# Optimization experiments

Measured on AMD Instinct MI355X. Metric: run time of the kernel, lower is better.

## Reference

```python
import jax, jax.numpy as jnp
import numpy as np

N_NODES = 50000
N_EDGES = 800000
IN_FEATS = 128
HIDDEN = 128
OUT_FEATS = 2
NUM_GRAPHS = 100


def xavier(key, shape):
    fan_in, fan_out = shape[1], shape[0]
    a = jnp.sqrt(6.0 / (fan_in + fan_out))
    return jax.random.uniform(key, shape, jnp.float32, -a, a)


def setup_inputs() -> dict:
    key = jax.random.key(0)
    ks = jax.random.split(key, 10)
    x = jax.random.normal(ks[0], (N_NODES, IN_FEATS), jnp.float32)
    edge_index = jax.random.randint(ks[1], (2, N_EDGES), 0, N_NODES, jnp.int64)
    edge_weight = jax.random.uniform(ks[2], (N_EDGES,), jnp.float32)
    batch = jnp.sort(jax.random.randint(ks[3], (N_NODES,), 0, NUM_GRAPHS, jnp.int64))
    return {
        "x": x,
        "edge_index": edge_index,
        "edge_weight": edge_weight,
        "batch": batch,
        "W1": xavier(ks[4], (HIDDEN, IN_FEATS)),
        "b1": jnp.zeros((HIDDEN,), jnp.float32),
        "W2": xavier(ks[5], (HIDDEN, HIDDEN)),
        "b2": jnp.zeros((HIDDEN,), jnp.float32),
        "lin1_w": xavier(ks[6], (IN_FEATS, HIDDEN)),
        "lin1_b": jnp.zeros((IN_FEATS,), jnp.float32),
        "lin2_w": xavier(ks[7], (OUT_FEATS, IN_FEATS)),
        "lin2_b": jnp.zeros((OUT_FEATS,), jnp.float32),
    }


def gcn_conv(x, row, col, ew, W, b, n_nodes):
    # PyG GCNConv: symmetric normalization with self-loops already included
    # deg[i] = sum of edge weights into node i
    deg = jax.ops.segment_sum(ew, col, num_segments=n_nodes)
    dinv = jnp.where(deg > 0, jax.lax.rsqrt(deg), 0.0)
    norm = dinv[row] * ew * dinv[col]                      # [E]
    h = x @ W.T                                            # [N, out]
    msg = norm[:, None] * h[row]                           # [E, out]
    out = jax.ops.segment_sum(msg, col, num_segments=n_nodes)
    return out + b


def reference(x, edge_index, edge_weight, batch, W1, b1, W2, b2,
              lin1_w, lin1_b, lin2_w, lin2_b):
    n = x.shape[0]
    # add self-loops with weight 1 (PyG default fill_value=1.0)
    loops = jnp.arange(n, dtype=edge_index.dtype)
    row = jnp.concatenate([edge_index[0], loops])
    col = jnp.concatenate([edge_index[1], loops])
    ew = jnp.concatenate([edge_weight, jnp.ones((n,), edge_weight.dtype)])

    h = jax.nn.relu(gcn_conv(x, row, col, ew, W1, b1, n))
    h = jax.nn.relu(gcn_conv(h, row, col, ew, W2, b2, n))

    # global_mean_pool over graph ids
    sums = jax.ops.segment_sum(h, batch, num_segments=NUM_GRAPHS)
    cnt = jax.ops.segment_sum(jnp.ones((n,), h.dtype), batch, num_segments=NUM_GRAPHS)
    g = sums / jnp.maximum(cnt, 1.0)[:, None]              # [G, hidden]

    # dropout is identity in eval mode
    g = jax.nn.relu(g @ lin1_w.T + lin1_b)
    return g @ lin2_w.T + lin2_b
```

## Files before the change

### kernel.cpp

```cpp
#include <hip/hip_runtime.h>


typedef unsigned long long ull;
typedef short bf16x8 __attribute__((ext_vector_type(8)));
typedef float f32x4 __attribute__((ext_vector_type(4)));

#define BCAP 2560
#define TILE_E 2048
#define NBINS 512

__device__ inline ushort f2bf(float f) {
    unsigned u = __float_as_uint(f);
    unsigned r = (u + 0x7FFF + ((u >> 16) & 1)) >> 16;
    return (ushort)r;
}
__device__ inline void bsplit(float f, ushort& h, ushort& l) {
    h = f2bf(f);
    float hf = __uint_as_float(((unsigned)h) << 16);
    l = f2bf(f - hf);
}
__device__ inline float bflo(unsigned g) { return __uint_as_float(g << 16); }
__device__ inline float bfhi(unsigned g) { return __uint_as_float(g & 0xffff0000u); }

__global__ void k_wsplit(const float* __restrict__ W1, const float* __restrict__ W2,
                         ushort* __restrict__ w1hi, ushort* __restrict__ w1lo,
                         ushort* __restrict__ w2hi, ushort* __restrict__ w2lo,
                         unsigned* __restrict__ cursor) {
    int i = blockIdx.x * blockDim.x + threadIdx.x;
    if (i < NBINS) cursor[i] = 0;
    if (i < 4096) {
        float4 v = ((const float4*)W1)[i];
        ushort4 h, l;
        bsplit(v.x, h.x, l.x); bsplit(v.y, h.y, l.y);
        bsplit(v.z, h.z, l.z); bsplit(v.w, h.w, l.w);
        ((ushort4*)w1hi)[i] = h; ((ushort4*)w1lo)[i] = l;
    } else if (i < 8192) {
        int j = i - 4096;
        float4 v = ((const float4*)W2)[j];
        ushort4 h, l;
        bsplit(v.x, h.x, l.x); bsplit(v.y, h.y, l.y);
        bsplit(v.z, h.z, l.z); bsplit(v.w, h.w, l.w);
        ((ushort4*)w2hi)[j] = h; ((ushort4*)w2lo)[j] = l;
    }
}

template <int AFP32, int POOL>
__device__ __forceinline__ void gemm_body(int blk, int t,
                                          const void* __restrict__ Xsrc,
                                          const ushort* __restrict__ whi,
                                          const ushort* __restrict__ wlo,
                                          ushort* __restrict__ Y, int N,
                                          const int* __restrict__ batch,
                                          const float* __restrict__ bias,
                                          float* __restrict__ pooled) {
    int lane = t & 63;
    int wave = t >> 6;
    int quad = lane >> 4;
    int l16  = lane & 15;
    int rowbase = blk * 128 + wave * 32;

    const f32x4 zero = {0.f, 0.f, 0.f, 0.f};
    f32x4 acc[2][8];
#pragma unroll
    for (int i = 0; i < 2; ++i)
#pragma unroll
        for (int j = 0; j < 8; ++j) acc[i][j] = zero;

#pragma unroll
    for (int kc = 0; kc < 128; kc += 32) {
        bf16x8 ah[2];
#pragma unroll
        for (int rt = 0; rt < 2; ++rt) {
            int r0 = rowbase + rt * 16 + l16;
            r0 = r0 < N ? r0 : N - 1;
            if (AFP32) {
                const float* ap = (const float*)Xsrc + (size_t)r0 * 128 + kc + quad * 8;
                float4 a0 = *(const float4*)ap;
                float4 a1 = *(const float4*)(ap + 4);
                bf16x8 v;
                v[0] = (short)f2bf(a0.x); v[1] = (short)f2bf(a0.y);
                v[2] = (short)f2bf(a0.z); v[3] = (short)f2bf(a0.w);
                v[4] = (short)f2bf(a1.x); v[5] = (short)f2bf(a1.y);
                v[6] = (short)f2bf(a1.z); v[7] = (short)f2bf(a1.w);
                ah[rt] = v;
            } else {
                ah[rt] = *(const bf16x8*)((const ushort*)Xsrc + (size_t)r0 * 128 + kc + quad * 8);
            }
        }
#pragma unroll
        for (int ct = 0; ct < 8; ++ct) {
            int boff = (ct * 16 + l16) * 128 + kc + quad * 8;
            bf16x8 bh = *(const bf16x8*)(whi + boff);
            bf16x8 bl = *(const bf16x8*)(wlo + boff);
#pragma unroll
            for (int rt = 0; rt < 2; ++rt) {
                acc[rt][ct] = __builtin_amdgcn_mfma_f32_16x16x32_bf16(ah[rt], bh, acc[rt][ct], 0, 0, 0);
                acc[rt][ct] = __builtin_amdgcn_mfma_f32_16x16x32_bf16(ah[rt], bl, acc[rt][ct], 0, 0, 0);
            }
        }
    }
    if constexpr (!POOL) {
#pragma unroll
        for (int rt = 0; rt < 2; ++rt) {
#pragma unroll
            for (int r = 0; r < 4; ++r) {
                int rowi = rowbase + rt * 16 + quad * 4 + r;
                if (rowi < N) {
                    ushort* yp = Y + (size_t)rowi * 128 + l16;
#pragma unroll
                    for (int ct = 0; ct < 8; ++ct)
                        yp[ct * 16] = f2bf(acc[rt][ct][r]);
                }
            }
        }
    } else {
        __shared__ ushort hb[128][132];
        __shared__ int bs[128];
        int n0 = blk * 128;
        if (t < 128) bs[t] = (n0 + t < N) ? batch[n0 + t] : -1;
#pragma unroll
        for (int ct = 0; ct < 8; ++ct) {
            float bb = bias[ct * 16 + l16];
#pragma unroll
            for (int rt = 0; rt < 2; ++rt)
#pragma unroll
                for (int r = 0; r < 4; ++r) {
                    int rl = wave * 32 + rt * 16 + quad * 4 + r;
                    hb[rl][ct * 16 + l16] = f2bf(fmaxf(acc[rt][ct][r] + bb, 0.f));
                }
        }
        __syncthreads();
        int col = t & 127, half = t >> 7;
        float a = 0.f; int cur = -2;
        for (int r = 0; r < 64; ++r) {
            int row = half * 64 + r;
            int g = bs[row];
            if (g != cur) {
                if (cur >= 0) atomicAdd(&pooled[cur * 128 + col], a);
                a = 0.f; cur = g;
            }
            if (g >= 0) a += __uint_as_float(((unsigned)hb[row][col]) << 16);
        }
        if (cur >= 0) atomicAdd(&pooled[cur * 128 + col], a);
    }
}

__global__ __launch_bounds__(256, 4) void k_front(const float* __restrict__ x,
                                                  const ushort* __restrict__ w1hi,
                                                  const ushort* __restrict__ w1lo,
                                                  ushort* __restrict__ h1, int N, int gb,
                                                  const int* __restrict__ row,
                                                  const int* __restrict__ col,
                                                  const float* __restrict__ ew,
                                                  ull* __restrict__ edata,
                                                  unsigned* __restrict__ cursor, int E) {
    __shared__ unsigned hist[NBINS];
    __shared__ unsigned gbase[NBINS];
    int b = blockIdx.x;
    if (b < gb) {
        gemm_body<1, 0>(b, threadIdx.x, x, w1hi, w1lo, h1, N, nullptr, nullptr, nullptr);
        return;
    }
    int t = threadIdx.x;
    int e0 = (b - gb) * TILE_E;
    hist[t] = 0; hist[t + 256] = 0;
    __syncthreads();
    int cl[TILE_E / 256];
#pragma unroll
    for (int i = 0; i < TILE_E / 256; ++i) {
        int e = e0 + i * 256 + t;
        int c = e < E ? col[e] : -1;
        cl[i] = c;
        if (c >= 0) atomicAdd(&hist[c >> 7], 1u);
    }
    __syncthreads();
#pragma unroll
    for (int i = 0; i < 2; ++i) {
        int bin = t + i * 256;
        unsigned h = hist[bin];
        if (h) gbase[bin] = atomicAdd(&cursor[bin], h);
    }
    __syncthreads();
#pragma unroll
    for (int i = 0; i < TILE_E / 256; ++i) {
        int c = cl[i];
        if (c < 0) continue;
        int e = e0 + i * 256 + t;
        unsigned q = (unsigned)rintf(ew[e] * 32768.0f);
        if (q > 32767u) q = 32767u;
        unsigned val = (q << 17) | (unsigned)row[e];
        int bk = c >> 7;
        unsigned off = atomicSub(&hist[bk], 1u) - 1u;
        unsigned dst = gbase[bk] + off;
        if (dst < (unsigned)BCAP)
            edata[(size_t)bk * BCAP + dst] = ((ull)(unsigned)c << 32) | (ull)val;
    }
}

__global__ __launch_bounds__(256) void k_slots(const ull* __restrict__ edata,
                                               const unsigned* __restrict__ cursor,
                                               ull* __restrict__ packed,
                                               unsigned* __restrict__ slots, int N) {
    __shared__ unsigned cnt[128];
    __shared__ unsigned ews[128];
    int b = blockIdx.x, t = threadIdx.x;
    if (t < 128) { cnt[t] = 0; ews[t] = 0; }
    __syncthreads();
    unsigned m = cursor[b];
    if (m > (unsigned)BCAP) m = BCAP;
    const ull* ed = edata + (size_t)b * BCAP;
    for (unsigned k = t; k < m; k += 256) {
        ull pv = ed[k];
        unsigned c = (unsigned)(pv >> 32);
        unsigned val = (unsigned)pv;
        unsigned clc = c & 127u;
        unsigned pos = atomicAdd(&cnt[clc], 1u);
        if (pos < 64u) slots[((size_t)c << 6) + pos] = val;
        atomicAdd(&ews[clc], val >> 17);
    }
    __syncthreads();
    if (t < 128) {
        int node = b * 128 + t;
        if (node < N) packed[node] = ((ull)cnt[t] << 32) | (ull)ews[t];
    }
}

__global__ __launch_bounds__(256, 4) void k_gemm2pool(const ushort* __restrict__ X,
                                                      const ushort* __restrict__ whi,
                                                      const ushort* __restrict__ wlo,
                                                      const int* __restrict__ batch,
                                                      const float* __restrict__ bias,
                                                      float* __restrict__ pooled, int N) {
    gemm_body<0, 1>(blockIdx.x, threadIdx.x, X, whi, wlo, nullptr, N, batch, bias, pooled);
}

template <int RELU>
__global__ __launch_bounds__(256) void k_agg(const ushort* __restrict__ H,
                                             ushort* __restrict__ Ob,
                                             const ull* __restrict__ packed,
                                             const unsigned* __restrict__ slots,
                                             const float* __restrict__ bias, int N) {
    int wid = __builtin_amdgcn_readfirstlane((blockIdx.x * blockDim.x + threadIdx.x) >> 6);
    int lane = threadIdx.x & 63;
    if (wid >= N) return;
    const unsigned* HU = (const unsigned*)H;
    const unsigned* PU = (const unsigned*)packed;
    const float kq = 3.0517578125e-5f;
    ull pk = packed[wid];
    int cnt = (int)(pk >> 32); cnt = cnt < 64 ? cnt : 64;
    float dsum = (float)(unsigned)(pk & 0xffffffffull) * kq;
    float dc = rsqrtf(1.0f + dsum);
    float dcs = dc * kq;
    const unsigned* SL = slots + ((size_t)wid << 6);
    unsigned gss = HU[(size_t)wid * 64 + lane];
    float ax = dc * dc * bflo(gss), ay = dc * dc * bfhi(gss);
    int c1 = cnt - 1;
    for (int j = 0; j < cnt; j += 8) {
        int j1 = j+1 < c1 ? j+1 : c1, j2 = j+2 < c1 ? j+2 : c1, j3 = j+3 < c1 ? j+3 : c1;
        int j4 = j+4 < c1 ? j+4 : c1, j5 = j+5 < c1 ? j+5 : c1, j6 = j+6 < c1 ? j+6 : c1;
        int j7 = j+7 < c1 ? j+7 : c1;
        unsigned p0 = SL[j],  p1 = SL[j1], p2 = SL[j2], p3 = SL[j3];
        unsigned p4 = SL[j4], p5 = SL[j5], p6 = SL[j6], p7 = SL[j7];
        unsigned s0 = p0 & 0x1FFFFu, s1 = p1 & 0x1FFFFu, s2 = p2 & 0x1FFFFu, s3 = p3 & 0x1FFFFu;
        unsigned s4 = p4 & 0x1FFFFu, s5 = p5 & 0x1FFFFu, s6 = p6 & 0x1FFFFu, s7 = p7 & 0x1FFFFu;
        float q0 = (float)(p0 >> 17);
        float q1 = j+1 < cnt ? (float)(p1 >> 17) : 0.f;
        float q2 = j+2 < cnt ? (float)(p2 >> 17) : 0.f;
        float q3 = j+3 < cnt ? (float)(p3 >> 17) : 0.f;
        float q4 = j+4 < cnt ? (float)(p4 >> 17) : 0.f;
        float q5 = j+5 < cnt ? (float)(p5 >> 17) : 0.f;
        float q6 = j+6 < cnt ? (float)(p6 >> 17) : 0.f;
        float q7 = j+7 < cnt ? (float)(p7 >> 17) : 0.f;
        float d0 = rsqrtf(1.f + (float)PU[2*s0] * kq);
        float d1 = rsqrtf(1.f + (float)PU[2*s1] * kq);
        float d2 = rsqrtf(1.f + (float)PU[2*s2] * kq);
        float d3 = rsqrtf(1.f + (float)PU[2*s3] * kq);
        float d4 = rsqrtf(1.f + (float)PU[2*s4] * kq);
        float d5 = rsqrtf(1.f + (float)PU[2*s5] * kq);
        float d6 = rsqrtf(1.f + (float)PU[2*s6] * kq);
        float d7 = rsqrtf(1.f + (float)PU[2*s7] * kq);
        float w0 = d0 * q0 * dcs, w1 = d1 * q1 * dcs, w2 = d2 * q2 * dcs, w3 = d3 * q3 * dcs;
        float w4 = d4 * q4 * dcs, w5 = d5 * q5 * dcs, w6 = d6 * q6 * dcs, w7 = d7 * q7 * dcs;
        unsigned g0 = HU[(size_t)s0 * 64 + lane];
        unsigned g1 = HU[(size_t)s1 * 64 + lane];
        unsigned g2 = HU[(size_t)s2 * 64 + lane];
        unsigned g3 = HU[(size_t)s3 * 64 + lane];
        unsigned g4 = HU[(size_t)s4 * 64 + lane];
        unsigned g5 = HU[(size_t)s5 * 64 + lane];
        unsigned g6 = HU[(size_t)s6 * 64 + lane];
        unsigned g7 = HU[(size_t)s7 * 64 + lane];
        ax += w0 * bflo(g0); ay += w0 * bfhi(g0);
        ax += w1 * bflo(g1); ay += w1 * bfhi(g1);
        ax += w2 * bflo(g2); ay += w2 * bfhi(g2);
        ax += w3 * bflo(g3); ay += w3 * bfhi(g3);
        ax += w4 * bflo(g4); ay += w4 * bfhi(g4);
        ax += w5 * bflo(g5); ay += w5 * bfhi(g5);
        ax += w6 * bflo(g6); ay += w6 * bfhi(g6);
        ax += w7 * bflo(g7); ay += w7 * bfhi(g7);
    }
    if constexpr (RELU) {
        float2 bb = ((const float2*)bias)[lane];
        ax = fmaxf(ax + bb.x, 0.f);
        ay = fmaxf(ay + bb.y, 0.f);
    }
    unsigned pkout = (unsigned)f2bf(ax) | ((unsigned)f2bf(ay) << 16);
    ((unsigned*)Ob)[(size_t)wid * 64 + lane] = pkout;
}

__global__ __launch_bounds__(128) void k_mlp(const float* __restrict__ pooled,
                                             const int* __restrict__ batch,
                                             const float* __restrict__ w1,
                                             const float* __restrict__ b1,
                                             const float* __restrict__ w2,
                                             const float* __restrict__ b2,
                                             float* __restrict__ out, int N, int G) {
    __shared__ float pl[128];
    __shared__ float h1[128];
    int g = blockIdx.x, t = threadIdx.x;
    int lo = 0, hi = N;
    while (lo < hi) { int m = (lo + hi) >> 1; if (batch[m] < g) lo = m + 1; else hi = m; }
    int s = lo;
    lo = s; hi = N;
    while (lo < hi) { int m = (lo + hi) >> 1; if (batch[m] < g + 1) lo = m + 1; else hi = m; }
    float cnt = (float)(lo - s);
    pl[t] = pooled[g * 128 + t] / fmaxf(cnt, 1.0f);
    __syncthreads();
    float sum = b1[t];
#pragma unroll 4
    for (int k = 0; k < 128; ++k) sum += w1[t * 128 + k] * pl[k];
    h1[t] = fmaxf(sum, 0.f);
    __syncthreads();
    if (t < 2) {
        float s2 = b2[t];
        for (int k = 0; k < 128; ++k) s2 += w2[t * 128 + k] * h1[k];
        out[g * 2 + t] = s2;
    }
}

extern "C" void kernel_launch(void* const* d_in, const int* in_sizes, int n_in,
                              void* d_out, int out_size, void* d_ws, size_t ws_size,
                              hipStream_t stream) {
    const float* x   = (const float*)d_in[0];
    const int*   ei  = (const int*)d_in[1];
    const float* ew  = (const float*)d_in[2];
    const int* batch = (const int*)d_in[3];
    const float* W1  = (const float*)d_in[4];
    const float* b1  = (const float*)d_in[5];
    const float* W2  = (const float*)d_in[6];
    const float* b2  = (const float*)d_in[7];
    const float* l1w = (const float*)d_in[8];
    const float* l1b = (const float*)d_in[9];
    const float* l2w = (const float*)d_in[10];
    const float* l2b = (const float*)d_in[11];
    float* out = (float*)d_out;

    const int E = in_sizes[2];
    const int N = in_sizes[3];
    const int G = out_size / 2;
    const int Npad = (N + 127) & ~127;
    const int nbk = (N + 127) >> 7;
    const int* row = ei;
    const int* col = ei + E;

    char* p = (char*)d_ws;
    auto alloc = [&](size_t bytes) -> void* {
        void* r = (void*)p;
        p += (bytes + 511) & ~(size_t)511;
        return r;
    };
    ull*     packed = (ull*)alloc((size_t)N * 8);
    unsigned* slots = (unsigned*)alloc((size_t)N * 64 * 4);
    ushort* w1hi  = (ushort*)alloc(16384 * 2);
    ushort* w1lo  = (ushort*)alloc(16384 * 2);
    ushort* w2hi  = (ushort*)alloc(16384 * 2);
    ushort* w2lo  = (ushort*)alloc(16384 * 2);
    ushort* h1    = (ushort*)alloc((size_t)Npad * 128 * 2);
    ushort* hagg  = (ushort*)alloc((size_t)Npad * 128 * 2);
    float* pooled = (float*)alloc((size_t)G * 128 * 4);
    ull*   edata  = (ull*)alloc((size_t)nbk * BCAP * 8);
    unsigned* cursor = (unsigned*)alloc(NBINS * 4);

    hipMemsetAsync(pooled, 0, (size_t)G * 128 * 4, stream);

    int nbS = (E + TILE_E - 1) / TILE_E;
    int gb = Npad / 128;
    int ab = ((size_t)N * 64 + 255) / 256;
    k_wsplit<<<32, 256, 0, stream>>>(W1, W2, w1hi, w1lo, w2hi, w2lo, cursor);
    k_front<<<gb + nbS, 256, 0, stream>>>(x, w1hi, w1lo, h1, N, gb,
                                          row, col, ew, edata, cursor, E);
    k_slots<<<nbk, 256, 0, stream>>>(edata, cursor, packed, slots, N);
    k_agg<1><<<ab, 256, 0, stream>>>(h1, hagg, packed, slots, b1, N);
    k_agg<0><<<ab, 256, 0, stream>>>(hagg, h1, packed, slots, nullptr, N);
    k_gemm2pool<<<gb, 256, 0, stream>>>(h1, w2hi, w2lo, batch, b2, pooled, N);
    k_mlp<<<G, 128, 0, stream>>>(pooled, batch, l1w, l1b, l2w, l2b, out, N, G);
}
```

Measured before the change: 237.8 us.

## Fuse second aggregation with GEMM2 and pooling; split weights inline

Merges the second aggregation pass, the second GEMM, the bias/ReLU step and mean-pool accumulation into one kernel. Aggregated rows are staged in an LDS tile and fed straight to MFMA, so the intermediate h1 round trip through global memory goes away. The weight split kernel is removed and each GEMM now splits fp32 weights into bf16 hi/lo inline, and the cursor reset is folded into the pooled memset. This cuts two launches and one global write/read of N×128 activations, but adds redundant per-block weight conversion work and gives the aggregation phase less parallelism (one wave handles 16 nodes serially).

Result: slower. 261.1 us (+9.8%).

```diff
diff --git a/kernel.cpp b/kernel.cpp
--- a/kernel.cpp
+++ b/kernel.cpp
@@ -8,6 +8,7 @@
 #define BCAP 2560
 #define TILE_E 2048
 #define NBINS 512
+#define APAD 136
 
 __device__ inline ushort f2bf(float f) {
     unsigned u = __float_as_uint(f);
@@ -22,37 +23,24 @@
 __device__ inline float bflo(unsigned g) { return __uint_as_float(g << 16); }
 __device__ inline float bfhi(unsigned g) { return __uint_as_float(g & 0xffff0000u); }
 
-__global__ void k_wsplit(const float* __restrict__ W1, const float* __restrict__ W2,
-                         ushort* __restrict__ w1hi, ushort* __restrict__ w1lo,
-                         ushort* __restrict__ w2hi, ushort* __restrict__ w2lo,
-                         unsigned* __restrict__ cursor) {
-    int i = blockIdx.x * blockDim.x + threadIdx.x;
-    if (i < NBINS) cursor[i] = 0;
-    if (i < 4096) {
-        float4 v = ((const float4*)W1)[i];
-        ushort4 h, l;
-        bsplit(v.x, h.x, l.x); bsplit(v.y, h.y, l.y);
-        bsplit(v.z, h.z, l.z); bsplit(v.w, h.w, l.w);
-        ((ushort4*)w1hi)[i] = h; ((ushort4*)w1lo)[i] = l;
-    } else if (i < 8192) {
-        int j = i - 4096;
-        float4 v = ((const float4*)W2)[j];
-        ushort4 h, l;
-        bsplit(v.x, h.x, l.x); bsplit(v.y, h.y, l.y);
-        bsplit(v.z, h.z, l.z); bsplit(v.w, h.w, l.w);
-        ((ushort4*)w2hi)[j] = h; ((ushort4*)w2lo)[j] = l;
-    }
-}
-
-template <int AFP32, int POOL>
-__device__ __forceinline__ void gemm_body(int blk, int t,
-                                          const void* __restrict__ Xsrc,
-                                          const ushort* __restrict__ whi,
-                                          const ushort* __restrict__ wlo,
-                                          ushort* __restrict__ Y, int N,
-                                          const int* __restrict__ batch,
-                                          const float* __restrict__ bias,
-                                          float* __restrict__ pooled) {
+__device__ __forceinline__ void wfrag(const float* __restrict__ wp, bf16x8& bh, bf16x8& bl) {
+    float4 w0 = *(const float4*)wp;
+    float4 w1 = *(const float4*)(wp + 4);
+    ushort h, l;
+    bsplit(w0.x, h, l); bh[0] = (short)h; bl[0] = (short)l;
+    bsplit(w0.y, h, l); bh[1] = (short)h; bl[1] = (short)l;
+    bsplit(w0.z, h, l); bh[2] = (short)h; bl[2] = (short)l;
+    bsplit(w0.w, h, l); bh[3] = (short)h; bl[3] = (short)l;
+    bsplit(w1.x, h, l); bh[4] = (short)h; bl[4] = (short)l;
+    bsplit(w1.y, h, l); bh[5] = (short)h; bl[5] = (short)l;
+    bsplit(w1.z, h, l); bh[6] = (short)h; bl[6] = (short)l;
+    bsplit(w1.w, h, l); bh[7] = (short)h; bl[7] = (short)l;
+}
+
+__device__ __forceinline__ void gemm1_body(int blk, int t,
+                                           const float* __restrict__ X,
+                                           const float* __restrict__ W,
+                                           ushort* __restrict__ Y, int N) {
     int lane = t & 63;
     int wave = t >> 6;
     int quad = lane >> 4;
@@ -73,25 +61,20 @@
         for (int rt = 0; rt < 2; ++rt) {
             int r0 = rowbase + rt * 16 + l16;
             r0 = r0 < N ? r0 : N - 1;
-            if (AFP32) {
-                const float* ap = (const float*)Xsrc + (size_t)r0 * 128 + kc + quad * 8;
-                float4 a0 = *(const float4*)ap;
-                float4 a1 = *(const float4*)(ap + 4);
-                bf16x8 v;
-                v[0] = (short)f2bf(a0.x); v[1] = (short)f2bf(a0.y);
-                v[2] = (short)f2bf(a0.z); v[3] = (short)f2bf(a0.w);
-                v[4] = (short)f2bf(a1.x); v[5] = (short)f2bf(a1.y);
-                v[6] = (short)f2bf(a1.z); v[7] = (short)f2bf(a1.w);
-                ah[rt] = v;
-            } else {
-                ah[rt] = *(const bf16x8*)((const ushort*)Xsrc + (size_t)r0 * 128 + kc + quad * 8);
-            }
+            const float* ap = X + (size_t)r0 * 128 + kc + quad * 8;
+            float4 a0 = *(const float4*)ap;
+            float4 a1 = *(const float4*)(ap + 4);
+            bf16x8 v;
+            v[0] = (short)f2bf(a0.x); v[1] = (short)f2bf(a0.y);
+            v[2] = (short)f2bf(a0.z); v[3] = (short)f2bf(a0.w);
+            v[4] = (short)f2bf(a1.x); v[5] = (short)f2bf(a1.y);
+            v[6] = (short)f2bf(a1.z); v[7] = (short)f2bf(a1.w);
+            ah[rt] = v;
         }
 #pragma unroll
         for (int ct = 0; ct < 8; ++ct) {
-            int boff = (ct * 16 + l16) * 128 + kc + quad * 8;
-            bf16x8 bh = *(const bf16x8*)(whi + boff);
-            bf16x8 bl = *(const bf16x8*)(wlo + boff);
+            bf16x8 bh, bl;
+            wfrag(W + (size_t)(ct * 16 + l16) * 128 + kc + quad * 8, bh, bl);
 #pragma unroll
             for (int rt = 0; rt < 2; ++rt) {
                 acc[rt][ct] = __builtin_amdgcn_mfma_f32_16x16x32_bf16(ah[rt], bh, acc[rt][ct], 0, 0, 0);
@@ -99,55 +82,23 @@
             }
         }
     }
-    if constexpr (!POOL) {
-#pragma unroll
-        for (int rt = 0; rt < 2; ++rt) {
-#pragma unroll
-            for (int r = 0; r < 4; ++r) {
-                int rowi = rowbase + rt * 16 + quad * 4 + r;
-                if (rowi < N) {
-                    ushort* yp = Y + (size_t)rowi * 128 + l16;
-#pragma unroll
-                    for (int ct = 0; ct < 8; ++ct)
-                        yp[ct * 16] = f2bf(acc[rt][ct][r]);
-                }
+#pragma unroll
+    for (int rt = 0; rt < 2; ++rt) {
+#pragma unroll
+        for (int r = 0; r < 4; ++r) {
+            int rowi = rowbase + rt * 16 + quad * 4 + r;
+            if (rowi < N) {
+                ushort* yp = Y + (size_t)rowi * 128 + l16;
+#pragma unroll
+                for (int ct = 0; ct < 8; ++ct)
+                    yp[ct * 16] = f2bf(acc[rt][ct][r]);
             }
         }
-    } else {
-        __shared__ ushort hb[128][132];
-        __shared__ int bs[128];
-        int n0 = blk * 128;
-        if (t < 128) bs[t] = (n0 + t < N) ? batch[n0 + t] : -1;
-#pragma unroll
-        for (int ct = 0; ct < 8; ++ct) {
-            float bb = bias[ct * 16 + l16];
-#pragma unroll
-            for (int rt = 0; rt < 2; ++rt)
-#pragma unroll
-                for (int r = 0; r < 4; ++r) {
-                    int rl = wave * 32 + rt * 16 + quad * 4 + r;
-                    hb[rl][ct * 16 + l16] = f2bf(fmaxf(acc[rt][ct][r] + bb, 0.f));
-                }
-        }
-        __syncthreads();
-        int col = t & 127, half = t >> 7;
-        float a = 0.f; int cur = -2;
-        for (int r = 0; r < 64; ++r) {
-            int row = half * 64 + r;
-            int g = bs[row];
-            if (g != cur) {
-                if (cur >= 0) atomicAdd(&pooled[cur * 128 + col], a);
-                a = 0.f; cur = g;
-            }
-            if (g >= 0) a += __uint_as_float(((unsigned)hb[row][col]) << 16);
-        }
-        if (cur >= 0) atomicAdd(&pooled[cur * 128 + col], a);
     }
 }
 
 __global__ __launch_bounds__(256, 4) void k_front(const float* __restrict__ x,
-                                                  const ushort* __restrict__ w1hi,
-                                                  const ushort* __restrict__ w1lo,
+                                                  const float* __restrict__ W1,
                                                   ushort* __restrict__ h1, int N, int gb,
                                                   const int* __restrict__ row,
                                                   const int* __restrict__ col,
@@ -158,7 +109,7 @@
     __shared__ unsigned gbase[NBINS];
     int b = blockIdx.x;
     if (b < gb) {
-        gemm_body<1, 0>(b, threadIdx.x, x, w1hi, w1lo, h1, N, nullptr, nullptr, nullptr);
+        gemm1_body(b, threadIdx.x, x, W1, h1, N);
         return;
     }
     int t = threadIdx.x;
@@ -225,26 +176,12 @@
     }
 }
 
-__global__ __launch_bounds__(256, 4) void k_gemm2pool(const ushort* __restrict__ X,
-                                                      const ushort* __restrict__ whi,
-                                                      const ushort* __restrict__ wlo,
-                                                      const int* __restrict__ batch,
-                                                      const float* __restrict__ bias,
-                                                      float* __restrict__ pooled, int N) {
-    gemm_body<0, 1>(blockIdx.x, threadIdx.x, X, whi, wlo, nullptr, N, batch, bias, pooled);
-}
-
-template <int RELU>
-__global__ __launch_bounds__(256) void k_agg(const ushort* __restrict__ H,
-                                             ushort* __restrict__ Ob,
-                                             const ull* __restrict__ packed,
-                                             const unsigned* __restrict__ slots,
-                                             const float* __restrict__ bias, int N) {
-    int wid = __builtin_amdgcn_readfirstlane((blockIdx.x * blockDim.x + threadIdx.x) >> 6);
-    int lane = threadIdx.x & 63;
-    if (wid >= N) return;
-    const unsigned* HU = (const unsigned*)H;
-    const unsigned* PU = (const unsigned*)packed;
+__device__ __forceinline__ void agg_node(int wid, int lane,
+                                         const unsigned* __restrict__ HU,
+                                         const unsigned* __restrict__ PU,
+                                         const ull* __restrict__ packed,
+                                         const unsigned* __restrict__ slots,
+                                         float& ax, float& ay) {
     const float kq = 3.0517578125e-5f;
     ull pk = packed[wid];
     int cnt = (int)(pk >> 32); cnt = cnt < 64 ? cnt : 64;
@@ -253,7 +190,7 @@
     float dcs = dc * kq;
     const unsigned* SL = slots + ((size_t)wid << 6);
     unsigned gss = HU[(size_t)wid * 64 + lane];
-    float ax = dc * dc * bflo(gss), ay = dc * dc * bfhi(gss);
+    ax = dc * dc * bflo(gss); ay = dc * dc * bfhi(gss);
     int c1 = cnt - 1;
     for (int j = 0; j < cnt; j += 8) {
         int j1 = j+1 < c1 ? j+1 : c1, j2 = j+2 < c1 ? j+2 : c1, j3 = j+3 < c1 ? j+3 : c1;
@@ -298,13 +235,85 @@
         ax += w6 * bflo(g6); ay += w6 * bfhi(g6);
         ax += w7 * bflo(g7); ay += w7 * bfhi(g7);
     }
-    if constexpr (RELU) {
-        float2 bb = ((const float2*)bias)[lane];
-        ax = fmaxf(ax + bb.x, 0.f);
-        ay = fmaxf(ay + bb.y, 0.f);
-    }
+}
+
+__global__ __launch_bounds__(256) void k_agg(const ushort* __restrict__ H,
+                                             ushort* __restrict__ Ob,
+                                             const ull* __restrict__ packed,
+                                             const unsigned* __restrict__ slots,
+                                             const float* __restrict__ bias, int N) {
+    int wid = __builtin_amdgcn_readfirstlane((blockIdx.x * blockDim.x + threadIdx.x) >> 6);
+    int lane = threadIdx.x & 63;
+    if (wid >= N) return;
+    float ax, ay;
+    agg_node(wid, lane, (const unsigned*)H, (const unsigned*)packed, packed, slots, ax, ay);
+    float2 bb = ((const float2*)bias)[lane];
+    ax = fmaxf(ax + bb.x, 0.f);
+    ay = fmaxf(ay + bb.y, 0.f);
     unsigned pkout = (unsigned)f2bf(ax) | ((unsigned)f2bf(ay) << 16);
     ((unsigned*)Ob)[(size_t)wid * 64 + lane] = pkout;
+}
+
+__global__ __launch_bounds__(512, 4) void k_aggpool(const ushort* __restrict__ H,
+                                                    const ull* __restrict__ packed,
+                                                    const unsigned* __restrict__ slots,
+                                                    const float* __restrict__ W2,
+                                                    const int* __restrict__ batch,
+                                                    const float* __restrict__ bias,
+                                                    float* __restrict__ pooled, int N) {
+    __shared__ ushort atile[128][APAD];
+    __shared__ int bs[128];
+    int t = threadIdx.x, blk = blockIdx.x;
+    int lane = t & 63, wave = t >> 6;
+    int quad = lane >> 4, l16 = lane & 15;
+    int n0 = blk * 128;
+    if (t < 128) bs[t] = (n0 + t < N) ? batch[n0 + t] : -1;
+    const unsigned* HU = (const unsigned*)H;
+    const unsigned* PU = (const unsigned*)packed;
+    for (int i = 0; i < 16; ++i) {
+        int r = wave * 16 + i;
+        int wid = n0 + r;
+        float ax = 0.f, ay = 0.f;
+        if (wid < N) agg_node(wid, lane, HU, PU, packed, slots, ax, ay);
+        *(unsigned*)&atile[r][lane * 2] = (unsigned)f2bf(ax) | ((unsigned)f2bf(ay) << 16);
+    }
+    const f32x4 zero = {0.f, 0.f, 0.f, 0.f};
+    f32x4 acc[8];
+#pragma unroll
+    for (int j = 0; j < 8; ++j) acc[j] = zero;
+#pragma unroll
+    for (int kc = 0; kc < 128; kc += 32) {
+        bf16x8 ah = *(const bf16x8*)&atile[wave * 16 + l16][kc + quad * 8];
+#pragma unroll
+        for (int ct = 0; ct < 8; ++ct) {
+            bf16x8 bh, bl;
+            wfrag(W2 + (size_t)(ct * 16 + l16) * 128 + kc + quad * 8, bh, bl);
+            acc[ct] = __builtin_amdgcn_mfma_f32_16x16x32_bf16(ah, bh, acc[ct], 0, 0, 0);
+            acc[ct] = __builtin_amdgcn_mfma_f32_16x16x32_bf16(ah, bl, acc[ct], 0, 0, 0);
+        }
+    }
+#pragma unroll
+    for (int ct = 0; ct < 8; ++ct) {
+        float bb = bias[ct * 16 + l16];
+#pragma unroll
+        for (int r = 0; r < 4; ++r) {
+            int rl = wave * 16 + quad * 4 + r;
+            atile[rl][ct * 16 + l16] = f2bf(fmaxf(acc[ct][r] + bb, 0.f));
+        }
+    }
+    __syncthreads();
+    int col = t & 127, qtr = t >> 7;
+    float a = 0.f; int cur = -2;
+    for (int r = 0; r < 32; ++r) {
+        int row = qtr * 32 + r;
+        int g = bs[row];
+        if (g != cur) {
+            if (cur >= 0) atomicAdd(&pooled[cur * 128 + col], a);
+            a = 0.f; cur = g;
+        }
+        if (g >= 0) a += __uint_as_float(((unsigned)atile[row][col]) << 16);
+    }
+    if (cur >= 0) atomicAdd(&pooled[cur * 128 + col], a);
 }
 
 __global__ __launch_bounds__(128) void k_mlp(const float* __restrict__ pooled,
@@ -370,27 +379,21 @@
     };
     ull*     packed = (ull*)alloc((size_t)N * 8);
     unsigned* slots = (unsigned*)alloc((size_t)N * 64 * 4);
-    ushort* w1hi  = (ushort*)alloc(16384 * 2);
-    ushort* w1lo  = (ushort*)alloc(16384 * 2);
-    ushort* w2hi  = (ushort*)alloc(16384 * 2);
-    ushort* w2lo  = (ushort*)alloc(16384 * 2);
     ushort* h1    = (ushort*)alloc((size_t)Npad * 128 * 2);
     ushort* hagg  = (ushort*)alloc((size_t)Npad * 128 * 2);
     float* pooled = (float*)alloc((size_t)G * 128 * 4);
+    unsigned* cursor = (unsigned*)alloc(NBINS * 4);
     ull*   edata  = (ull*)alloc((size_t)nbk * BCAP * 8);
-    unsigned* cursor = (unsigned*)alloc(NBINS * 4);
-
-    hipMemsetAsync(pooled, 0, (size_t)G * 128 * 4, stream);
+
+    hipMemsetAsync(pooled, 0, (size_t)G * 128 * 4 + NBINS * 4, stream);
 
     int nbS = (E + TILE_E - 1) / TILE_E;
     int gb = Npad / 128;
     int ab = ((size_t)N * 64 + 255) / 256;
-    k_wsplit<<<32, 256, 0, stream>>>(W1, W2, w1hi, w1lo, w2hi, w2lo, cursor);
-    k_front<<<gb + nbS, 256, 0, stream>>>(x, w1hi, w1lo, h1, N, gb,
+    k_front<<<gb + nbS, 256, 0, stream>>>(x, W1, h1, N, gb,
                                           row, col, ew, edata, cursor, E);
     k_slots<<<nbk, 256, 0, stream>>>(edata, cursor, packed, slots, N);
-    k_agg<1><<<ab, 256, 0, stream>>>(h1, hagg, packed, slots, b1, N);
-    k_agg<0><<<ab, 256, 0, stream>>>(hagg, h1, packed, slots, nullptr, N);
-    k_gemm2pool<<<gb, 256, 0, stream>>>(h1, w2hi, w2lo, batch, b2, pooled, N);
+    k_agg<<<ab, 256, 0, stream>>>(h1, hagg, packed, slots, b1, N);
+    k_aggpool<<<gb, 512, 0, stream>>>(hagg, packed, slots, W2, batch, b2, pooled, N);
     k_mlp<<<G, 128, 0, stream>>>(pooled, batch, l1w, l1b, l2w, l2b, out, N, G);
 }
```
